# Kernel tuning notes

Measured on AMD Instinct MI355X. Metric: run time of the kernel, lower is better.

## Reference

```python
import jax, jax.numpy as jnp
import numpy as np


def setup_inputs() -> dict:
    key = jax.random.key(0)
    k1, k2, k3 = jax.random.split(key, 3)
    C, H, W = 64, 512, 512
    D, K = 128, 3
    input = jax.random.normal(k1, (C, H, W), dtype=jnp.float32)
    # He-style init as in the module
    kernels = jax.random.normal(k2, (D, C, K, K), dtype=jnp.float32) * jnp.sqrt(2.0 / (C * K * K))
    biases = jax.random.normal(k3, (D, H - K + 1, W - K + 1), dtype=jnp.float32)
    return {"input": input, "kernels": kernels, "biases": biases}


def reference(input, kernels, biases):
    # valid 2D cross-correlation summed over input channels, plus per-pixel bias
    # input: [C,H,W], kernels: [D,C,k,k], biases: [D,H-k+1,W-k+1]
    x = input[None]  # [1,C,H,W]
    out = jax.lax.conv_general_dilated(
        x, kernels,
        window_strides=(1, 1),
        padding="VALID",
        dimension_numbers=("NCHW", "OIHW", "NCHW"),
    )[0]  # [D,H-k+1,W-k+1]; lax conv is cross-correlation, matching correlate2d
    return out + biases
```

## Files before the change

kernel.cpp:

```cpp
#include <hip/hip_runtime.h>
#include <hip/hip_bf16.h>

#define C_IN 64
#define H_IN 512
#define W_IN 512
#define D_OUT 128
#define OH 510
#define OW 510

typedef __bf16 bf16x8 __attribute__((ext_vector_type(8)));
typedef float  f32x4  __attribute__((ext_vector_type(4)));
typedef float  f32x2  __attribute__((ext_vector_type(2)));

#define TIN_ELEMS (H_IN * W_IN * C_IN)
#define TIN_BYTES ((size_t)TIN_ELEMS * 2)
#define WT_BYTES  (9 * D_OUT * C_IN * 2)
#define WS_NEEDED (TIN_BYTES + WT_BYTES)

__global__ void prep_weights(const float* __restrict__ w, __bf16* __restrict__ wt) {
    int i = blockIdx.x * blockDim.x + threadIdx.x;
    if (i >= 9 * D_OUT * C_IN) return;
    int c    = i & 63;
    int d    = (i >> 6) & 127;
    int kpos = i >> 13;
    wt[i] = (__bf16)w[((d * C_IN) + c) * 9 + kpos];
}

__global__ __launch_bounds__(256, 4)
void transpose_in(const float* __restrict__ in, __bf16* __restrict__ tin) {
    __shared__ float ls[32 * 257];
    const int b    = blockIdx.x;
    const int y    = b >> 1;
    const int px0  = (b & 1) << 8;
    const int t    = threadIdx.x;
    const int wave = t >> 6;
    const int lane = t & 63;

    for (int cc = 0; cc < 2; cc++) {
        if (cc) __syncthreads();
#pragma unroll
        for (int j = 0; j < 8; j++) {
            const int cl = wave * 8 + j;
            f32x4 v = *(const f32x4*)&in[(cc * 32 + cl) * (H_IN * W_IN) + y * W_IN + px0 + lane * 4];
            *(f32x4*)&ls[cl * 257 + lane * 4] = v;
        }
        __syncthreads();
        const int oct = t & 3;
        const int pxw = t >> 2;
#pragma unroll
        for (int pass = 0; pass < 4; pass++) {
            const int pxl = pass * 64 + pxw;
            bf16x8 v;
#pragma unroll
            for (int j = 0; j < 8; j++)
                v[j] = (__bf16)ls[(oct * 8 + j) * 257 + pxl];
            *(bf16x8*)&tin[((size_t)(y * W_IN) + px0 + pxl) * C_IN + cc * 32 + oct * 8] = v;
        }
    }
}

__global__ __launch_bounds__(256, 2)
void conv_main(const __bf16* __restrict__ tin, const __bf16* __restrict__ wt,
               const float* __restrict__ bias, float* __restrict__ out) {
    __shared__ float lo[128 * 68];
    const int b    = blockIdx.x;
    const int y    = b >> 3;
    const int xt   = b & 7;
    const int x0   = (xt == 7) ? (OW - 64) : (xt * 64);
    const int wave = threadIdx.x >> 6;
    const int lane = threadIdx.x & 63;
    const int l15  = lane & 15;
    const int quad = lane >> 4;

    bf16x8 wf[9][2][2];
#pragma unroll
    for (int kpos = 0; kpos < 9; kpos++)
#pragma unroll
        for (int ch = 0; ch < 2; ch++)
#pragma unroll
            for (int dg = 0; dg < 2; dg++) {
                wf[kpos][ch][dg] = *(const bf16x8*)(wt + kpos * (D_OUT * C_IN)
                                        + (wave * 32 + dg * 16 + l15) * C_IN
                                        + ch * 32 + quad * 8);
                asm volatile("" : "+v"(wf[kpos][ch][dg]));
            }

    f32x4 acc[4][2];
#pragma unroll
    for (int pxg = 0; pxg < 4; pxg++)
#pragma unroll
        for (int dg = 0; dg < 2; dg++)
            acc[pxg][dg] = (f32x4){0.f, 0.f, 0.f, 0.f};

#pragma unroll
    for (int kpos = 0; kpos < 9; kpos++) {
        const int ky = kpos / 3, kx = kpos % 3;
#pragma unroll
        for (int ch = 0; ch < 2; ch++) {
            const __bf16* base = tin + ((size_t)(y + ky) * W_IN + x0 + kx) * C_IN
                                     + ch * 32 + quad * 8;
#pragma unroll
            for (int pxg = 0; pxg < 4; pxg++) {
                bf16x8 pf = *(const bf16x8*)(base + (pxg * 16 + l15) * C_IN);
                acc[pxg][0] = __builtin_amdgcn_mfma_f32_16x16x32_bf16(pf, wf[kpos][ch][0], acc[pxg][0], 0, 0, 0);
                acc[pxg][1] = __builtin_amdgcn_mfma_f32_16x16x32_bf16(pf, wf[kpos][ch][1], acc[pxg][1], 0, 0, 0);
            }
        }
    }

#pragma unroll
    for (int pxg = 0; pxg < 4; pxg++)
#pragma unroll
        for (int dg = 0; dg < 2; dg++) {
            const int dl = wave * 32 + dg * 16 + l15;
            *(f32x4*)&lo[dl * 68 + pxg * 16 + quad * 4] = acc[pxg][dg];
        }
    __syncthreads();
    const int xq   = threadIdx.x & 15;
    const int dgrp = threadIdx.x >> 4;
#pragma unroll
    for (int i = 0; i < 8; i++) {
        const int d = dgrp * 8 + i;
        f32x4 v = *(const f32x4*)&lo[d * 68 + xq * 4];
        const size_t o = (size_t)d * (OH * OW) + (size_t)y * OW + x0 + xq * 4;
        f32x2 b0 = *(const f32x2*)&bias[o];
        f32x2 b1 = *(const f32x2*)&bias[o + 2];
        f32x2 r0 = {v[0] + b0[0], v[1] + b0[1]};
        f32x2 r1 = {v[2] + b1[0], v[3] + b1[1]};
        *(f32x2*)&out[o]     = r0;
        *(f32x2*)&out[o + 2] = r1;
    }
}

#define PXT 64
#define TCOL 66
#define TCPAD 72

__global__ __launch_bounds__(256, 4)
void conv_bias_fallback(const float* __restrict__ in, const __bf16* __restrict__ wt,
                        const float* __restrict__ bias, float* __restrict__ out) {
    __shared__ __bf16 tile[3 * TCOL * TCPAD];
    const int b  = blockIdx.x;
    const int y  = b >> 3;
    const int x0 = (b & 7) * PXT;
    const int tid = threadIdx.x;
    for (int idx = tid; idx < 3 * TCOL * C_IN; idx += 256) {
        int col = idx % TCOL;
        int t   = idx / TCOL;
        int r   = t % 3;
        int c   = t / 3;
        int gx  = x0 + col;
        if (gx > W_IN - 1) gx = W_IN - 1;
        tile[(r * TCOL + col) * TCPAD + c] = (__bf16)in[(c * H_IN + (y + r)) * W_IN + gx];
    }
    __syncthreads();
    const int wave = tid >> 6, lane = tid & 63;
    const int l15 = lane & 15, quad = lane >> 4;
    const int px_base = wave * 16;
    f32x4 acc[8];
#pragma unroll
    for (int i = 0; i < 8; i++) acc[i] = (f32x4){0.f, 0.f, 0.f, 0.f};
#pragma unroll
    for (int kpos = 0; kpos < 9; kpos++) {
        const int ky = kpos / 3, kx = kpos % 3;
#pragma unroll
        for (int ch = 0; ch < 2; ch++) {
            const int c0 = ch * 32;
            bf16x8 bfrag = *(const bf16x8*)&tile[(ky * TCOL + px_base + l15 + kx) * TCPAD + c0 + quad * 8];
            const __bf16* aptr = wt + (size_t)kpos * D_OUT * C_IN + l15 * C_IN + c0 + quad * 8;
#pragma unroll
            for (int ds = 0; ds < 8; ds++) {
                bf16x8 afrag = *(const bf16x8*)(aptr + ds * 16 * C_IN);
                acc[ds] = __builtin_amdgcn_mfma_f32_16x16x32_bf16(afrag, bfrag, acc[ds], 0, 0, 0);
            }
        }
    }
    const int gx = x0 + px_base + l15;
    if (gx < OW) {
#pragma unroll
        for (int ds = 0; ds < 8; ds++) {
            const int dbase = ds * 16 + quad * 4;
#pragma unroll
            for (int r = 0; r < 4; r++) {
                const size_t o = ((size_t)(dbase + r) * OH + y) * OW + gx;
                out[o] = acc[ds][r] + bias[o];
            }
        }
    }
}

extern "C" void kernel_launch(void* const* d_in, const int* in_sizes, int n_in,
                              void* d_out, int out_size, void* d_ws, size_t ws_size,
                              hipStream_t stream) {
    const float* in   = (const float*)d_in[0];
    const float* w    = (const float*)d_in[1];
    const float* bias = (const float*)d_in[2];
    float* out = (float*)d_out;

    if (ws_size >= WS_NEEDED) {
        __bf16* tin = (__bf16*)d_ws;
        __bf16* wt  = (__bf16*)((char*)d_ws + TIN_BYTES);
        prep_weights<<<(9 * D_OUT * C_IN + 255) / 256, 256, 0, stream>>>(w, wt);
        transpose_in<<<H_IN * 2, 256, 0, stream>>>(in, tin);
        conv_main<<<OH * 8, 256, 0, stream>>>(tin, wt, bias, out);
    } else {
        __bf16* wt = (__bf16*)d_ws;
        prep_weights<<<(9 * D_OUT * C_IN + 255) / 256, 256, 0, stream>>>(w, wt);
        conv_bias_fallback<<<OH * 8, 256, 0, stream>>>(in, wt, bias, out);
    }
}
```

Measured before the change: 476.6 us.

## Retile conv_main to 32 output channels by 256 pixels with weights staged in LDS

Each block now computes a 32-channel by 256-pixel tile instead of 128 channels by 64 pixels. Its weights are staged once into XOR-swizzled shared memory rather than held as 36 bf16x8 register fragments. That frees registers so occupancy can rise from 2 to 4 blocks per CU. Bias values are prefetched before the MFMA loop to hide their latency, and the LDS buffer is reused for the output transpose. In exchange, each input pixel row is fetched by four channel-tile blocks instead of one, which raises L2 traffic on the transposed input, and extra LDS reads occur per kpos.

New measurement: 416.6 us. -12.6%, faster.

```diff
diff --git a/kernel.cpp b/kernel.cpp
--- a/kernel.cpp
+++ b/kernel.cpp
@@ -59,31 +59,47 @@
     }
 }
 
-__global__ __launch_bounds__(256, 2)
+#define BPX 256
+#define LO_STRIDE 260
+
+__global__ __launch_bounds__(256, 4)
 void conv_main(const __bf16* __restrict__ tin, const __bf16* __restrict__ wt,
                const float* __restrict__ bias, float* __restrict__ out) {
-    __shared__ float lo[128 * 68];
+    __shared__ __align__(16) char smem[9 * 32 * 64 * 2];
+    __bf16* lw = (__bf16*)smem;
+    float*  lo = (float*)smem;
+
     const int b    = blockIdx.x;
+    const int dt   = b & 3;
+    const int xt   = (b >> 2) & 1;
     const int y    = b >> 3;
-    const int xt   = b & 7;
-    const int x0   = (xt == 7) ? (OW - 64) : (xt * 64);
-    const int wave = threadIdx.x >> 6;
-    const int lane = threadIdx.x & 63;
+    const int d0   = dt << 5;
+    const int x0   = xt ? (OW - BPX) : 0;
+
+    const int t    = threadIdx.x;
+    const int wave = t >> 6;
+    const int lane = t & 63;
     const int l15  = lane & 15;
     const int quad = lane >> 4;
 
-    bf16x8 wf[9][2][2];
-#pragma unroll
-    for (int kpos = 0; kpos < 9; kpos++)
-#pragma unroll
-        for (int ch = 0; ch < 2; ch++)
-#pragma unroll
-            for (int dg = 0; dg < 2; dg++) {
-                wf[kpos][ch][dg] = *(const bf16x8*)(wt + kpos * (D_OUT * C_IN)
-                                        + (wave * 32 + dg * 16 + l15) * C_IN
-                                        + ch * 32 + quad * 8);
-                asm volatile("" : "+v"(wf[kpos][ch][dg]));
-            }
+    {
+        const int dl  = t >> 3, oc = t & 7;
+        const int ocs = (oc ^ (dl & 7)) * 8;
+#pragma unroll
+        for (int kpos = 0; kpos < 9; kpos++) {
+            bf16x8 v = *(const bf16x8*)(wt + kpos * (D_OUT * C_IN) + (d0 + dl) * C_IN + oc * 8);
+            *(bf16x8*)&lw[(kpos * 32 + dl) * 64 + ocs] = v;
+        }
+    }
+    __syncthreads();
+
+    f32x2 bvals[16];
+    const size_t ob = (size_t)(d0 + wave * 8) * (OH * OW) + (size_t)y * OW + x0 + lane * 4;
+#pragma unroll
+    for (int i = 0; i < 8; i++) {
+        bvals[2 * i]     = *(const f32x2*)&bias[ob + (size_t)i * (OH * OW)];
+        bvals[2 * i + 1] = *(const f32x2*)&bias[ob + (size_t)i * (OH * OW) + 2];
+    }
 
     f32x4 acc[4][2];
 #pragma unroll
@@ -92,41 +108,41 @@
         for (int dg = 0; dg < 2; dg++)
             acc[pxg][dg] = (f32x4){0.f, 0.f, 0.f, 0.f};
 
+    const __bf16* tb = tin + ((size_t)y * W_IN + x0 + wave * 64) * C_IN + quad * 8;
 #pragma unroll
     for (int kpos = 0; kpos < 9; kpos++) {
         const int ky = kpos / 3, kx = kpos % 3;
 #pragma unroll
         for (int ch = 0; ch < 2; ch++) {
-            const __bf16* base = tin + ((size_t)(y + ky) * W_IN + x0 + kx) * C_IN
-                                     + ch * 32 + quad * 8;
+            const int us = (((ch * 4 + quad) ^ (l15 & 7)) * 8);
+            bf16x8 w0 = *(const bf16x8*)&lw[(kpos * 32 + l15) * 64 + us];
+            bf16x8 w1 = *(const bf16x8*)&lw[(kpos * 32 + 16 + l15) * 64 + us];
+            const __bf16* base = tb + ((size_t)ky * W_IN + kx) * C_IN + ch * 32;
 #pragma unroll
             for (int pxg = 0; pxg < 4; pxg++) {
                 bf16x8 pf = *(const bf16x8*)(base + (pxg * 16 + l15) * C_IN);
-                acc[pxg][0] = __builtin_amdgcn_mfma_f32_16x16x32_bf16(pf, wf[kpos][ch][0], acc[pxg][0], 0, 0, 0);
-                acc[pxg][1] = __builtin_amdgcn_mfma_f32_16x16x32_bf16(pf, wf[kpos][ch][1], acc[pxg][1], 0, 0, 0);
+                acc[pxg][0] = __builtin_amdgcn_mfma_f32_16x16x32_bf16(pf, w0, acc[pxg][0], 0, 0, 0);
+                acc[pxg][1] = __builtin_amdgcn_mfma_f32_16x16x32_bf16(pf, w1, acc[pxg][1], 0, 0, 0);
             }
         }
     }
 
 #pragma unroll
+    for (int i = 0; i < 16; i++) asm volatile("" : "+v"(bvals[i]));
+
+    __syncthreads();
+#pragma unroll
     for (int pxg = 0; pxg < 4; pxg++)
 #pragma unroll
-        for (int dg = 0; dg < 2; dg++) {
-            const int dl = wave * 32 + dg * 16 + l15;
-            *(f32x4*)&lo[dl * 68 + pxg * 16 + quad * 4] = acc[pxg][dg];
-        }
-    __syncthreads();
-    const int xq   = threadIdx.x & 15;
-    const int dgrp = threadIdx.x >> 4;
+        for (int dg = 0; dg < 2; dg++)
+            *(f32x4*)&lo[(dg * 16 + l15) * LO_STRIDE + wave * 64 + pxg * 16 + quad * 4] = acc[pxg][dg];
+    __syncthreads();
 #pragma unroll
     for (int i = 0; i < 8; i++) {
-        const int d = dgrp * 8 + i;
-        f32x4 v = *(const f32x4*)&lo[d * 68 + xq * 4];
-        const size_t o = (size_t)d * (OH * OW) + (size_t)y * OW + x0 + xq * 4;
-        f32x2 b0 = *(const f32x2*)&bias[o];
-        f32x2 b1 = *(const f32x2*)&bias[o + 2];
-        f32x2 r0 = {v[0] + b0[0], v[1] + b0[1]};
-        f32x2 r1 = {v[2] + b1[0], v[3] + b1[1]};
+        f32x4 v = *(const f32x4*)&lo[(wave * 8 + i) * LO_STRIDE + lane * 4];
+        const size_t o = ob + (size_t)i * (OH * OW);
+        f32x2 r0 = { v[0] + bvals[2 * i][0],     v[1] + bvals[2 * i][1] };
+        f32x2 r1 = { v[2] + bvals[2 * i + 1][0], v[3] + bvals[2 * i + 1][1] };
         *(f32x2*)&out[o]     = r0;
         *(f32x2*)&out[o + 2] = r1;
     }
```
